# Performance work log

Measured on AMD Instinct MI355X. Metric: run time of the kernel, lower is better.

Reference implementation:

```python
import jax, jax.numpy as jnp
import numpy as np

N_NODES = 50000


def _add_self_loops(edge_index, num_nodes):
    loop = jnp.arange(num_nodes, dtype=edge_index.dtype)
    src = jnp.concatenate([edge_index[0], loop])
    dst = jnp.concatenate([edge_index[1], loop])
    return src, dst


def _gcn_norm(src, dst, num_nodes, dtype):
    # symmetric normalization: deg^{-1/2}[src] * deg^{-1/2}[dst]
    deg = jax.ops.segment_sum(jnp.ones_like(dst, dtype=dtype), dst,
                              num_segments=num_nodes)
    dinv = jnp.where(deg > 0, jax.lax.rsqrt(deg), 0.0).astype(dtype)
    return dinv[src] * dinv[dst]


def _gcn_conv(x, src, dst, norm, W, b, num_nodes):
    h = x @ W                                  # [N, out]
    msg = norm[:, None] * h[src]               # [E', out] gather
    agg = jax.ops.segment_sum(msg, dst, num_segments=num_nodes)  # scatter-add
    return agg + b


def setup_inputs() -> dict:
    key = jax.random.key(0)
    k1, k2, k3, k4 = jax.random.split(key, 4)
    x = jax.random.normal(k1, (N_NODES, 64), dtype=jnp.float32)
    edge_index = jax.random.randint(k2, (2, 800000), 0, N_NODES, dtype=jnp.int64)
    W1 = jax.random.normal(k3, (64, 64), dtype=jnp.float32) * (1.0 / np.sqrt(64))
    b1 = jnp.zeros((64,), dtype=jnp.float32)
    W2 = jax.random.normal(k4, (64, 37), dtype=jnp.float32) * (1.0 / np.sqrt(64))
    b2 = jnp.zeros((37,), dtype=jnp.float32)
    return {"x": x, "edge_index": edge_index, "W1": W1, "b1": b1,
            "W2": W2, "b2": b2}


def reference(x, edge_index, W1, b1, W2, b2):
    n = x.shape[0]
    src, dst = _add_self_loops(edge_index, n)
    norm = _gcn_norm(src, dst, n, x.dtype)
    h = _gcn_conv(x, src, dst, norm, W1, b1, n)
    h = jax.nn.relu(h)
    out = _gcn_conv(h, src, dst, norm, W2, b2, n)
    return out
```

## Files before the change

kernel.cpp:

```cpp
#include <hip/hip_runtime.h>

#define F_OUT 37
#define BSHIFT 7
#define BSIZE 128
#define CAP 3072
#define STAGE_CAP 3072
#define XS_STRIDE 68


__global__ void init_gcur(int* __restrict__ gcur, int nb) {
    int t = blockIdx.x * blockDim.x + threadIdx.x;
    if (t < nb) gcur[t * 16] = t * CAP;
}

__global__ __launch_bounds__(256) void bucketA(const int* __restrict__ src,
                                               const int* __restrict__ dst,
                                               int E, int C, int nb,
                                               int* __restrict__ gcur,
                                               unsigned* __restrict__ bedge) {
    __shared__ unsigned stage[STAGE_CAP];
    __shared__ int lcnt[400];
    __shared__ int lbase[400];
    int t = threadIdx.x;
    int e0 = blockIdx.x * C;
    int cnt = E - e0; if (cnt > C) cnt = C; if (cnt <= 0) return;

    for (int i = t; i < nb; i += 256) lcnt[i] = 0;
    __syncthreads();
    for (int i = t; i < cnt; i += 256) {
        int s = src[e0 + i], d = dst[e0 + i];
        int b = d >> BSHIFT;
        atomicAdd(&lcnt[b], 1);
        stage[i] = ((unsigned)b << 23) | ((unsigned)(d & (BSIZE - 1)) << 16) | (unsigned)s;
    }
    __syncthreads();
    for (int i = t; i < nb; i += 256)
        lbase[i] = lcnt[i] ? atomicAdd(&gcur[i * 16], lcnt[i]) : 0;
    __syncthreads();
    for (int i = t; i < nb; i += 256) lcnt[i] = 0;
    __syncthreads();
    for (int i = t; i < cnt; i += 256) {
        unsigned w = stage[i];
        int b = w >> 23;
        int pos = lbase[b] + atomicAdd(&lcnt[b], 1);
        bedge[pos] = w & 0x7FFFFFu;
    }
}

__global__ __launch_bounds__(512) void scan_buckets(const int* __restrict__ gcur,
                                                    int nb, int E, int n,
                                                    int* __restrict__ bstart,
                                                    int* __restrict__ rowptr) {
    __shared__ int s[512];
    int t = threadIdx.x;
    int v = (t < nb) ? (gcur[t * 16] - t * CAP) : 0;
    s[t] = v;
    __syncthreads();
    for (int o = 1; o < 512; o <<= 1) {
        int a = (t >= o) ? s[t - o] : 0;
        __syncthreads();
        s[t] += a;
        __syncthreads();
    }
    if (t < nb) bstart[t] = s[t] - v;
    if (t == 0) rowptr[n] = E;
}

__global__ __launch_bounds__(256) void bucketB(const unsigned* __restrict__ bedge,
                                               const int* __restrict__ gcur,
                                               const int* __restrict__ bstart,
                                               int n,
                                               int* __restrict__ rowptr,
                                               int* __restrict__ srcIdx,
                                               float* __restrict__ dinv) {
    __shared__ int hcnt[BSIZE], hoff[BSIZE], hcur[BSIZE], tmp[BSIZE];
    int b = blockIdx.x;
    int t = threadIdx.x;
    int cntb = gcur[b * 16] - b * CAP;
    int base = bstart[b];
    const unsigned* ed = bedge + (size_t)b * CAP;

    if (t < BSIZE) { hcnt[t] = 0; hcur[t] = 0; }
    __syncthreads();
    for (int i = t; i < cntb; i += 256) atomicAdd(&hcnt[ed[i] >> 16], 1);
    __syncthreads();
    if (t < BSIZE) tmp[t] = hcnt[t];
    __syncthreads();
    for (int o = 1; o < BSIZE; o <<= 1) {
        int a = (t < BSIZE && t >= o) ? tmp[t - o] : 0;
        __syncthreads();
        if (t < BSIZE) tmp[t] += a;
        __syncthreads();
    }
    if (t < BSIZE) hoff[t] = tmp[t] - hcnt[t];
    __syncthreads();
    int node = b * BSIZE + t;
    if (t < BSIZE && node < n) {
        rowptr[node] = base + hoff[t];
        dinv[node] = rsqrtf(1.0f + (float)hcnt[t]);
    }
    for (int i = t; i < cntb; i += 256) {
        unsigned w = ed[i];
        int dloc = w >> 16;
        int pos = base + hoff[dloc] + atomicAdd(&hcur[dloc], 1);
        srcIdx[pos] = (int)(w & 0xFFFFu);
    }
}


#define MICRO_STEP(XI, ACC)                                                    \
    do {                                                                       \
        ACC[0] += XI.x * w0.x; ACC[1] += XI.x * w0.y;                          \
        ACC[2] += XI.x * w0.z; ACC[3] += XI.x * w0.w;                          \
        ACC[0] += XI.y * w1.x; ACC[1] += XI.y * w1.y;                          \
        ACC[2] += XI.y * w1.z; ACC[3] += XI.y * w1.w;                          \
        ACC[0] += XI.z * w2.x; ACC[1] += XI.z * w2.y;                          \
        ACC[2] += XI.z * w2.z; ACC[3] += XI.z * w2.w;                          \
        ACC[0] += XI.w * w3.x; ACC[1] += XI.w * w3.y;                          \
        ACC[2] += XI.w * w3.z; ACC[3] += XI.w * w3.w;                          \
    } while (0)

__global__ __launch_bounds__(256, 4) void gemm64(const float* __restrict__ x,
                                                 const float* __restrict__ W,
                                                 const float* __restrict__ dinv,
                                                 float* __restrict__ hs, int n) {
    __shared__ float Xs[64 * XS_STRIDE];
    __shared__ float Ws[64 * 64];
    int t = threadIdx.x;
    const float4* W4 = (const float4*)W;
#pragma unroll
    for (int i = 0; i < 4; ++i)
        ((float4*)Ws)[t + i * 256] = W4[t + i * 256];
    int row0 = blockIdx.x * 64;
#pragma unroll
    for (int i = 0; i < 4; ++i) {
        int idx = i * 256 + t;
        int r = idx >> 4, k4 = idx & 15;
        int grow = row0 + r;
        float4 v = (grow < n) ? ((const float4*)x)[(size_t)grow * 16 + k4]
                              : make_float4(0.f, 0.f, 0.f, 0.f);
        *(float4*)&Xs[r * XS_STRIDE + k4 * 4] = v;
    }
    __syncthreads();

    int tc = t & 15, tr = t >> 4;
    float a0[4] = {0.f, 0.f, 0.f, 0.f};
    float a1[4] = {0.f, 0.f, 0.f, 0.f};
    float a2[4] = {0.f, 0.f, 0.f, 0.f};
    float a3[4] = {0.f, 0.f, 0.f, 0.f};

#pragma unroll 2
    for (int k = 0; k < 64; k += 4) {
        float4 w0 = *(const float4*)&Ws[(k + 0) * 64 + 4 * tc];
        float4 w1 = *(const float4*)&Ws[(k + 1) * 64 + 4 * tc];
        float4 w2 = *(const float4*)&Ws[(k + 2) * 64 + 4 * tc];
        float4 w3 = *(const float4*)&Ws[(k + 3) * 64 + 4 * tc];
        float4 x0 = *(const float4*)&Xs[(4 * tr + 0) * XS_STRIDE + k];
        float4 x1 = *(const float4*)&Xs[(4 * tr + 1) * XS_STRIDE + k];
        float4 x2 = *(const float4*)&Xs[(4 * tr + 2) * XS_STRIDE + k];
        float4 x3 = *(const float4*)&Xs[(4 * tr + 3) * XS_STRIDE + k];
        MICRO_STEP(x0, a0);
        MICRO_STEP(x1, a1);
        MICRO_STEP(x2, a2);
        MICRO_STEP(x3, a3);
    }

    {
        int row = row0 + 4 * tr;
        if (row < n) {
            float dd = dinv[row];
            ((float4*)hs)[(size_t)row * 16 + tc] =
                make_float4(a0[0] * dd, a0[1] * dd, a0[2] * dd, a0[3] * dd);
        }
        if (row + 1 < n) {
            float dd = dinv[row + 1];
            ((float4*)hs)[(size_t)(row + 1) * 16 + tc] =
                make_float4(a1[0] * dd, a1[1] * dd, a1[2] * dd, a1[3] * dd);
        }
        if (row + 2 < n) {
            float dd = dinv[row + 2];
            ((float4*)hs)[(size_t)(row + 2) * 16 + tc] =
                make_float4(a2[0] * dd, a2[1] * dd, a2[2] * dd, a2[3] * dd);
        }
        if (row + 3 < n) {
            float dd = dinv[row + 3];
            ((float4*)hs)[(size_t)(row + 3) * 16 + tc] =
                make_float4(a3[0] * dd, a3[1] * dd, a3[2] * dd, a3[3] * dd);
        }
    }
}

__global__ __launch_bounds__(256, 4) void gemm37(const float* __restrict__ t2,
                                                 const float* __restrict__ W,
                                                 const float* __restrict__ bias,
                                                 float* __restrict__ out, int n) {
    __shared__ float Xs[64 * XS_STRIDE];
    __shared__ float Ws[64 * 64];
    int t = threadIdx.x;
    for (int i = t; i < 64 * 64; i += 256) {
        int k = i >> 6, c = i & 63;
        Ws[i] = (c < F_OUT) ? W[k * F_OUT + c] : 0.f;
    }
    int row0 = blockIdx.x * 64;
#pragma unroll
    for (int i = 0; i < 4; ++i) {
        int idx = i * 256 + t;
        int r = idx >> 4, k4 = idx & 15;
        int grow = row0 + r;
        float4 v = (grow < n) ? ((const float4*)t2)[(size_t)grow * 16 + k4]
                              : make_float4(0.f, 0.f, 0.f, 0.f);
        *(float4*)&Xs[r * XS_STRIDE + k4 * 4] = v;
    }
    __syncthreads();

    int tc = t & 15, tr = t >> 4;
    float a0[4] = {0.f, 0.f, 0.f, 0.f};
    float a1[4] = {0.f, 0.f, 0.f, 0.f};
    float a2[4] = {0.f, 0.f, 0.f, 0.f};
    float a3[4] = {0.f, 0.f, 0.f, 0.f};

#pragma unroll 2
    for (int k = 0; k < 64; k += 4) {
        float4 w0 = *(const float4*)&Ws[(k + 0) * 64 + 4 * tc];
        float4 w1 = *(const float4*)&Ws[(k + 1) * 64 + 4 * tc];
        float4 w2 = *(const float4*)&Ws[(k + 2) * 64 + 4 * tc];
        float4 w3 = *(const float4*)&Ws[(k + 3) * 64 + 4 * tc];
        float4 x0 = *(const float4*)&Xs[(4 * tr + 0) * XS_STRIDE + k];
        float4 x1 = *(const float4*)&Xs[(4 * tr + 1) * XS_STRIDE + k];
        float4 x2 = *(const float4*)&Xs[(4 * tr + 2) * XS_STRIDE + k];
        float4 x3 = *(const float4*)&Xs[(4 * tr + 3) * XS_STRIDE + k];
        MICRO_STEP(x0, a0);
        MICRO_STEP(x1, a1);
        MICRO_STEP(x2, a2);
        MICRO_STEP(x3, a3);
    }

    if (4 * tc < F_OUT) {
        int c0 = 4 * tc;
        float b0 = bias[c0];
        float b1v = (c0 + 1 < F_OUT) ? bias[c0 + 1] : 0.f;
        float b2v = (c0 + 2 < F_OUT) ? bias[c0 + 2] : 0.f;
        float b3v = (c0 + 3 < F_OUT) ? bias[c0 + 3] : 0.f;
#define STORE_ROW(ACC, R)                                                      \
        do {                                                                   \
            int row = row0 + 4 * tr + (R);                                     \
            if (row < n) {                                                     \
                float* o = &out[(size_t)row * F_OUT + c0];                     \
                o[0] = ACC[0] + b0;                                            \
                if (c0 + 1 < F_OUT) o[1] = ACC[1] + b1v;                       \
                if (c0 + 2 < F_OUT) o[2] = ACC[2] + b2v;                       \
                if (c0 + 3 < F_OUT) o[3] = ACC[3] + b3v;                       \
            }                                                                  \
        } while (0)
        STORE_ROW(a0, 0);
        STORE_ROW(a1, 1);
        STORE_ROW(a2, 2);
        STORE_ROW(a3, 3);
#undef STORE_ROW
    }
}


template <bool RELU>
__global__ void agg_kernel(const int* __restrict__ rowptr, const int* __restrict__ srcIdx,
                           const float* __restrict__ dinv, const float* __restrict__ hs,
                           const float* __restrict__ bias, float* __restrict__ outp,
                           int n) {
    int t = blockIdx.x * blockDim.x + threadIdx.x;
    int d = t >> 4;
    int sub = t & 15;
    if (d >= n) return;
    const float4* h4 = (const float4*)hs;
    float4 acc = h4[(size_t)d * 16 + sub];
    int beg = rowptr[d], end = rowptr[d + 1];
    int j = beg;
    for (; j + 4 <= end; j += 4) {
        int s0 = srcIdx[j],     s1 = srcIdx[j + 1];
        int s2 = srcIdx[j + 2], s3 = srcIdx[j + 3];
        float4 v0 = h4[(size_t)s0 * 16 + sub];
        float4 v1 = h4[(size_t)s1 * 16 + sub];
        float4 v2 = h4[(size_t)s2 * 16 + sub];
        float4 v3 = h4[(size_t)s3 * 16 + sub];
        acc.x += (v0.x + v1.x) + (v2.x + v3.x);
        acc.y += (v0.y + v1.y) + (v2.y + v3.y);
        acc.z += (v0.z + v1.z) + (v2.z + v3.z);
        acc.w += (v0.w + v1.w) + (v2.w + v3.w);
    }
    for (; j < end; ++j) {
        int s = srcIdx[j];
        float4 v = h4[(size_t)s * 16 + sub];
        acc.x += v.x; acc.y += v.y; acc.z += v.z; acc.w += v.w;
    }
    float dd = dinv[d];
    float4 r;
    if (RELU) {
        float4 b = ((const float4*)bias)[sub];
        r.x = fmaxf(acc.x * dd + b.x, 0.f) * dd;
        r.y = fmaxf(acc.y * dd + b.y, 0.f) * dd;
        r.z = fmaxf(acc.z * dd + b.z, 0.f) * dd;
        r.w = fmaxf(acc.w * dd + b.w, 0.f) * dd;
    } else {
        r.x = acc.x * dd; r.y = acc.y * dd; r.z = acc.z * dd; r.w = acc.w * dd;
    }
    ((float4*)outp)[(size_t)d * 16 + sub] = r;
}

extern "C" void kernel_launch(void* const* d_in, const int* in_sizes, int n_in,
                              void* d_out, int out_size, void* d_ws, size_t ws_size,
                              hipStream_t stream) {
    const float* x  = (const float*)d_in[0];
    const int*   ei = (const int*)d_in[1];
    const float* W1 = (const float*)d_in[2];
    const float* b1 = (const float*)d_in[3];
    const float* W2 = (const float*)d_in[4];
    const float* b2 = (const float*)d_in[5];
    float* out = (float*)d_out;

    const int n = in_sizes[0] / 64;
    const int E = in_sizes[1] / 2;
    const int* src = ei;
    const int* dst = ei + E;

    const int nb = (n + BSIZE - 1) >> BSHIFT;
    const int nblkA = (E + STAGE_CAP - 1) / STAGE_CAP;
    const int C = (E + nblkA - 1) / nblkA;

    char* p = (char*)d_ws;
    int*   gcur   = (int*)p;   p += (size_t)nb * 16 * 4;
    int*   bstart = (int*)p;   p += (size_t)((nb + 3) & ~3) * 4;
    int*   rowptr = (int*)p;   p += (size_t)(n + 4) * 4;
    float* dinv   = (float*)p; p += (size_t)n * 4;
    int*   srcIdx = (int*)p;   p += (size_t)E * 4;
    float* hs     = (float*)p; p += (size_t)n * 64 * 4;
    float* h1s    = (float*)p; p += (size_t)n * 64 * 4;
    unsigned* bedge = (unsigned*)hs;
    float* t2     = hs;

    init_gcur<<<(nb + 255) / 256, 256, 0, stream>>>(gcur, nb);
    bucketA<<<nblkA, 256, 0, stream>>>(src, dst, E, C, nb, gcur, bedge);
    scan_buckets<<<1, 512, 0, stream>>>(gcur, nb, E, n, bstart, rowptr);
    bucketB<<<nb, 256, 0, stream>>>(bedge, gcur, bstart, n, rowptr, srcIdx, dinv);

    const int gemmBlocks = (n + 63) / 64;
    const int aggBlocks  = (n * 16 + 255) / 256;

    gemm64<<<gemmBlocks, 256, 0, stream>>>(x, W1, dinv, hs, n);
    agg_kernel<true><<<aggBlocks, 256, 0, stream>>>(rowptr, srcIdx, dinv, hs, b1, h1s, n);

    agg_kernel<false><<<aggBlocks, 256, 0, stream>>>(rowptr, srcIdx, dinv, h1s, nullptr, t2, n);
    gemm37<<<gemmBlocks, 256, 0, stream>>>(t2, W2, b2, out, n);
}
```

Baseline: 137.4 us.

## Reorder layer-2 as GEMM-then-aggregate on padded 40-wide features with shuffled index loads

The second layer now projects to 37 outputs (padded to 40) before aggregation instead of aggregating 64-wide features and then multiplying. This cuts the gathered bytes per edge in the second sparse pass. Both aggregation kernels also load 16 source indices cooperatively per 16-lane group and broadcast them with shuffles, so more gathers are in flight at once. Six of the 16 lanes sit idle in the 40-wide aggregation, and the index buffer is padded so the 16-wide index reads stay in bounds.

```diff
diff --git a/kernel.cpp b/kernel.cpp
--- a/kernel.cpp
+++ b/kernel.cpp
@@ -190,10 +190,9 @@
     }
 }
 
-__global__ __launch_bounds__(256, 4) void gemm37(const float* __restrict__ t2,
+__global__ __launch_bounds__(256, 4) void gemm37(const float* __restrict__ h1s,
                                                  const float* __restrict__ W,
-                                                 const float* __restrict__ bias,
-                                                 float* __restrict__ out, int n) {
+                                                 float* __restrict__ g40, int n) {
     __shared__ float Xs[64 * XS_STRIDE];
     __shared__ float Ws[64 * 64];
     int t = threadIdx.x;
@@ -207,7 +206,7 @@
         int idx = i * 256 + t;
         int r = idx >> 4, k4 = idx & 15;
         int grow = row0 + r;
-        float4 v = (grow < n) ? ((const float4*)t2)[(size_t)grow * 16 + k4]
+        float4 v = (grow < n) ? ((const float4*)h1s)[(size_t)grow * 16 + k4]
                               : make_float4(0.f, 0.f, 0.f, 0.f);
         *(float4*)&Xs[r * XS_STRIDE + k4 * 4] = v;
     }
@@ -235,74 +234,145 @@
         MICRO_STEP(x3, a3);
     }
 
-    if (4 * tc < F_OUT) {
-        int c0 = 4 * tc;
-        float b0 = bias[c0];
-        float b1v = (c0 + 1 < F_OUT) ? bias[c0 + 1] : 0.f;
-        float b2v = (c0 + 2 < F_OUT) ? bias[c0 + 2] : 0.f;
-        float b3v = (c0 + 3 < F_OUT) ? bias[c0 + 3] : 0.f;
-#define STORE_ROW(ACC, R)                                                      \
-        do {                                                                   \
-            int row = row0 + 4 * tr + (R);                                     \
-            if (row < n) {                                                     \
-                float* o = &out[(size_t)row * F_OUT + c0];                     \
-                o[0] = ACC[0] + b0;                                            \
-                if (c0 + 1 < F_OUT) o[1] = ACC[1] + b1v;                       \
-                if (c0 + 2 < F_OUT) o[2] = ACC[2] + b2v;                       \
-                if (c0 + 3 < F_OUT) o[3] = ACC[3] + b3v;                       \
-            }                                                                  \
-        } while (0)
-        STORE_ROW(a0, 0);
-        STORE_ROW(a1, 1);
-        STORE_ROW(a2, 2);
-        STORE_ROW(a3, 3);
-#undef STORE_ROW
-    }
-}
-
-
-template <bool RELU>
-__global__ void agg_kernel(const int* __restrict__ rowptr, const int* __restrict__ srcIdx,
-                           const float* __restrict__ dinv, const float* __restrict__ hs,
-                           const float* __restrict__ bias, float* __restrict__ outp,
-                           int n) {
+    if (tc < 10) {
+        int row = row0 + 4 * tr;
+        if (row < n)
+            ((float4*)g40)[(size_t)row * 10 + tc] =
+                make_float4(a0[0], a0[1], a0[2], a0[3]);
+        if (row + 1 < n)
+            ((float4*)g40)[(size_t)(row + 1) * 10 + tc] =
+                make_float4(a1[0], a1[1], a1[2], a1[3]);
+        if (row + 2 < n)
+            ((float4*)g40)[(size_t)(row + 2) * 10 + tc] =
+                make_float4(a2[0], a2[1], a2[2], a2[3]);
+        if (row + 3 < n)
+            ((float4*)g40)[(size_t)(row + 3) * 10 + tc] =
+                make_float4(a3[0], a3[1], a3[2], a3[3]);
+    }
+}
+
+
+#define ACCP4(A, B, C, D)                                                      \
+    acc.x += (A.x + B.x) + (C.x + D.x);                                        \
+    acc.y += (A.y + B.y) + (C.y + D.y);                                        \
+    acc.z += (A.z + B.z) + (C.z + D.z);                                        \
+    acc.w += (A.w + B.w) + (C.w + D.w);
+
+__global__ void agg64_kernel(const int* __restrict__ rowptr,
+                             const int* __restrict__ srcIdx,
+                             const float* __restrict__ dinv,
+                             const float* __restrict__ hs,
+                             const float* __restrict__ bias,
+                             float* __restrict__ outp, int n) {
     int t = blockIdx.x * blockDim.x + threadIdx.x;
-    int d = t >> 4;
-    int sub = t & 15;
+    int d = t >> 4, sub = t & 15;
     if (d >= n) return;
+    int gbase = threadIdx.x & 48;
     const float4* h4 = (const float4*)hs;
     float4 acc = h4[(size_t)d * 16 + sub];
     int beg = rowptr[d], end = rowptr[d + 1];
     int j = beg;
-    for (; j + 4 <= end; j += 4) {
-        int s0 = srcIdx[j],     s1 = srcIdx[j + 1];
-        int s2 = srcIdx[j + 2], s3 = srcIdx[j + 3];
-        float4 v0 = h4[(size_t)s0 * 16 + sub];
-        float4 v1 = h4[(size_t)s1 * 16 + sub];
-        float4 v2 = h4[(size_t)s2 * 16 + sub];
-        float4 v3 = h4[(size_t)s3 * 16 + sub];
-        acc.x += (v0.x + v1.x) + (v2.x + v3.x);
-        acc.y += (v0.y + v1.y) + (v2.y + v3.y);
-        acc.z += (v0.z + v1.z) + (v2.z + v3.z);
-        acc.w += (v0.w + v1.w) + (v2.w + v3.w);
+#define LD64(Q) float4 v##Q = h4[(size_t)__shfl(myIdx, gbase + Q) * 16 + sub];
+    for (; j + 16 <= end; j += 16) {
+        int myIdx = srcIdx[j + sub];
+        LD64(0) LD64(1) LD64(2) LD64(3) LD64(4) LD64(5) LD64(6) LD64(7)
+        LD64(8) LD64(9) LD64(10) LD64(11) LD64(12) LD64(13) LD64(14) LD64(15)
+        ACCP4(v0, v1, v2, v3) ACCP4(v4, v5, v6, v7)
+        ACCP4(v8, v9, v10, v11) ACCP4(v12, v13, v14, v15)
+    }
+    if (j + 8 <= end) {
+        int myIdx = srcIdx[j + sub];
+        LD64(0) LD64(1) LD64(2) LD64(3) LD64(4) LD64(5) LD64(6) LD64(7)
+        ACCP4(v0, v1, v2, v3) ACCP4(v4, v5, v6, v7)
+        j += 8;
+    }
+    if (j + 4 <= end) {
+        int s0 = srcIdx[j], s1 = srcIdx[j + 1], s2 = srcIdx[j + 2], s3 = srcIdx[j + 3];
+        float4 v0 = h4[(size_t)s0 * 16 + sub], v1 = h4[(size_t)s1 * 16 + sub];
+        float4 v2 = h4[(size_t)s2 * 16 + sub], v3 = h4[(size_t)s3 * 16 + sub];
+        ACCP4(v0, v1, v2, v3)
+        j += 4;
+    }
+    for (; j < end; ++j) {
+        float4 v = h4[(size_t)srcIdx[j] * 16 + sub];
+        acc.x += v.x; acc.y += v.y; acc.z += v.z; acc.w += v.w;
+    }
+#undef LD64
+    float dd = dinv[d];
+    float4 b = ((const float4*)bias)[sub];
+    float4 r;
+    r.x = fmaxf(acc.x * dd + b.x, 0.f) * dd;
+    r.y = fmaxf(acc.y * dd + b.y, 0.f) * dd;
+    r.z = fmaxf(acc.z * dd + b.z, 0.f) * dd;
+    r.w = fmaxf(acc.w * dd + b.w, 0.f) * dd;
+    ((float4*)outp)[(size_t)d * 16 + sub] = r;
+}
+
+__global__ void agg40_kernel(const int* __restrict__ rowptr,
+                             const int* __restrict__ srcIdx,
+                             const float* __restrict__ dinv,
+                             const float* __restrict__ g40,
+                             const float* __restrict__ bias,
+                             float* __restrict__ out, int n) {
+    int t = blockIdx.x * blockDim.x + threadIdx.x;
+    int d = t >> 4, sub = t & 15;
+    if (d >= n) return;
+    int gbase = threadIdx.x & 48;
+    bool act = sub < 10;
+    const float4* g4 = (const float4*)g40;
+    float4 acc = make_float4(0.f, 0.f, 0.f, 0.f);
+    if (act) acc = g4[(size_t)d * 10 + sub];
+    int beg = rowptr[d], end = rowptr[d + 1];
+    int j = beg;
+#define SH40(Q) int s##Q = __shfl(myIdx, gbase + Q);
+#define G40(Q)  float4 v##Q = g4[(size_t)s##Q * 10 + sub];
+    for (; j + 16 <= end; j += 16) {
+        int myIdx = srcIdx[j + sub];
+        SH40(0) SH40(1) SH40(2) SH40(3) SH40(4) SH40(5) SH40(6) SH40(7)
+        SH40(8) SH40(9) SH40(10) SH40(11) SH40(12) SH40(13) SH40(14) SH40(15)
+        if (act) {
+            G40(0) G40(1) G40(2) G40(3) G40(4) G40(5) G40(6) G40(7)
+            G40(8) G40(9) G40(10) G40(11) G40(12) G40(13) G40(14) G40(15)
+            ACCP4(v0, v1, v2, v3) ACCP4(v4, v5, v6, v7)
+            ACCP4(v8, v9, v10, v11) ACCP4(v12, v13, v14, v15)
+        }
+    }
+    if (j + 8 <= end) {
+        int myIdx = srcIdx[j + sub];
+        SH40(0) SH40(1) SH40(2) SH40(3) SH40(4) SH40(5) SH40(6) SH40(7)
+        if (act) {
+            G40(0) G40(1) G40(2) G40(3) G40(4) G40(5) G40(6) G40(7)
+            ACCP4(v0, v1, v2, v3) ACCP4(v4, v5, v6, v7)
+        }
+        j += 8;
+    }
+    if (j + 4 <= end) {
+        int s0 = srcIdx[j], s1 = srcIdx[j + 1], s2 = srcIdx[j + 2], s3 = srcIdx[j + 3];
+        if (act) {
+            float4 v0 = g4[(size_t)s0 * 10 + sub], v1 = g4[(size_t)s1 * 10 + sub];
+            float4 v2 = g4[(size_t)s2 * 10 + sub], v3 = g4[(size_t)s3 * 10 + sub];
+            ACCP4(v0, v1, v2, v3)
+        }
+        j += 4;
     }
     for (; j < end; ++j) {
         int s = srcIdx[j];
-        float4 v = h4[(size_t)s * 16 + sub];
-        acc.x += v.x; acc.y += v.y; acc.z += v.z; acc.w += v.w;
-    }
-    float dd = dinv[d];
-    float4 r;
-    if (RELU) {
-        float4 b = ((const float4*)bias)[sub];
-        r.x = fmaxf(acc.x * dd + b.x, 0.f) * dd;
-        r.y = fmaxf(acc.y * dd + b.y, 0.f) * dd;
-        r.z = fmaxf(acc.z * dd + b.z, 0.f) * dd;
-        r.w = fmaxf(acc.w * dd + b.w, 0.f) * dd;
-    } else {
-        r.x = acc.x * dd; r.y = acc.y * dd; r.z = acc.z * dd; r.w = acc.w * dd;
-    }
-    ((float4*)outp)[(size_t)d * 16 + sub] = r;
+        if (act) {
+            float4 v = g4[(size_t)s * 10 + sub];
+            acc.x += v.x; acc.y += v.y; acc.z += v.z; acc.w += v.w;
+        }
+    }
+#undef SH40
+#undef G40
+    if (act) {
+        float dd = dinv[d];
+        int c0 = 4 * sub;
+        float* o = &out[(size_t)d * F_OUT + c0];
+        o[0] = acc.x * dd + bias[c0];
+        if (c0 + 1 < F_OUT) o[1] = acc.y * dd + bias[c0 + 1];
+        if (c0 + 2 < F_OUT) o[2] = acc.z * dd + bias[c0 + 2];
+        if (c0 + 3 < F_OUT) o[3] = acc.w * dd + bias[c0 + 3];
+    }
 }
 
 extern "C" void kernel_launch(void* const* d_in, const int* in_sizes, int n_in,
@@ -330,11 +400,11 @@
     int*   bstart = (int*)p;   p += (size_t)((nb + 3) & ~3) * 4;
     int*   rowptr = (int*)p;   p += (size_t)(n + 4) * 4;
     float* dinv   = (float*)p; p += (size_t)n * 4;
-    int*   srcIdx = (int*)p;   p += (size_t)E * 4;
+    int*   srcIdx = (int*)p;   p += (size_t)(E + 16) * 4;
     float* hs     = (float*)p; p += (size_t)n * 64 * 4;
     float* h1s    = (float*)p; p += (size_t)n * 64 * 4;
     unsigned* bedge = (unsigned*)hs;
-    float* t2     = hs;
+    float* g40    = hs;
 
     init_gcur<<<(nb + 255) / 256, 256, 0, stream>>>(gcur, nb);
     bucketA<<<nblkA, 256, 0, stream>>>(src, dst, E, C, nb, gcur, bedge);
@@ -345,8 +415,8 @@
     const int aggBlocks  = (n * 16 + 255) / 256;
 
     gemm64<<<gemmBlocks, 256, 0, stream>>>(x, W1, dinv, hs, n);
-    agg_kernel<true><<<aggBlocks, 256, 0, stream>>>(rowptr, srcIdx, dinv, hs, b1, h1s, n);
-
-    agg_kernel<false><<<aggBlocks, 256, 0, stream>>>(rowptr, srcIdx, dinv, h1s, nullptr, t2, n);
-    gemm37<<<gemmBlocks, 256, 0, stream>>>(t2, W2, b2, out, n);
-}
+    agg64_kernel<<<aggBlocks, 256, 0, stream>>>(rowptr, srcIdx, dinv, hs, b1, h1s, n);
+
+    gemm37<<<gemmBlocks, 256, 0, stream>>>(h1s, W2, g40, n);
+    agg40_kernel<<<aggBlocks, 256, 0, stream>>>(rowptr, srcIdx, dinv, g40, b2, out, n);
+}
```

After: 133.8 us. 1.03x faster.
